# Optimization experiments

Hardware: AMD Instinct MI355X
Metric: run time of the kernel (lower is better)

## Reference

```python
import jax, jax.numpy as jnp
import numpy as np

N = 4096        # num nodes
D_IN = 256      # input_dim
E_DIM = 512     # quantum_dim
H = 8           # num_heads
HD = E_DIM // H # head_dim
N_EDGES = 131072
N_CELL_TYPES = 50


def setup_inputs() -> dict:
    key = jax.random.key(0)
    ks = jax.random.split(key, 12)
    s_in = 1.0 / np.sqrt(D_IN)
    s_e = 1.0 / np.sqrt(E_DIM)
    f32 = jnp.float32
    return {
        "node_features": jax.random.normal(ks[0], (N, D_IN), f32),
        "edge_index": jax.random.randint(ks[1], (2, N_EDGES), 0, N),
        "cell_types": jax.random.randint(ks[2], (N,), 0, N_CELL_TYPES),
        "Wq": (jax.random.normal(ks[3], (E_DIM, D_IN), f32) * s_in),
        "bq": jnp.zeros((E_DIM,), f32),
        "Wk": (jax.random.normal(ks[4], (E_DIM, D_IN), f32) * s_in),
        "bk": jnp.zeros((E_DIM,), f32),
        "Wv": (jax.random.normal(ks[5], (E_DIM, D_IN), f32) * s_in),
        "bv": jnp.zeros((E_DIM,), f32),
        "bio": (jax.random.normal(ks[6], (E_DIM, E_DIM), f32) * s_e),
        "cell_emb": jax.random.normal(ks[7], (N_CELL_TYPES, E_DIM), f32),
        "in_proj_w": (jax.random.normal(ks[8], (3 * E_DIM, E_DIM), f32) * s_e),
        "in_proj_b": jnp.zeros((3 * E_DIM,), f32),
        "out_w": (jax.random.normal(ks[9], (E_DIM, E_DIM), f32) * s_e),
        "out_b": jnp.zeros((E_DIM,), f32),
    }


def reference(node_features, edge_index, cell_types, Wq, bq, Wk, bk, Wv, bv,
              bio, cell_emb, in_proj_w, in_proj_b, out_w, out_b):
    # projections [N, E_DIM]
    Q = node_features @ Wq.T + bq
    K = node_features @ Wk.T + bk
    V = node_features @ Wv.T + bv
    # biological constraint mixing
    Q = Q @ bio
    K = K @ bio.T
    # cell-type embedding offsets
    ce = cell_emb[cell_types]  # [N, E_DIM]
    Q = Q + 0.1 * ce
    K = K + 0.1 * ce
    # graph edge-masked attention scores [N, N]
    scores = (Q @ K.T) / np.float32(np.sqrt(E_DIM))
    mask = jnp.zeros((N, N), jnp.bool_).at[edge_index[0], edge_index[1]].set(True)
    scores = jnp.where(mask, scores, jnp.float32(-1e9))
    attn = jax.nn.softmax(scores, axis=-1)
    # standard MHA (entanglement_layer) in eval mode (no dropout)
    wq_i, wk_i, wv_i = jnp.split(in_proj_w, 3, axis=0)
    bq_i, bk_i, bv_i = jnp.split(in_proj_b, 3)
    q = (Q @ wq_i.T + bq_i).reshape(N, H, HD).transpose(1, 0, 2)  # [H,N,HD]
    k = (K @ wk_i.T + bk_i).reshape(N, H, HD).transpose(1, 0, 2)
    v = (V @ wv_i.T + bv_i).reshape(N, H, HD).transpose(1, 0, 2)
    a2 = jax.nn.softmax(jnp.einsum('hnd,hmd->hnm', q, k) / np.float32(np.sqrt(HD)), axis=-1)
    o = jnp.einsum('hnm,hmd->hnd', a2, v).transpose(1, 0, 2).reshape(N, E_DIM)
    attended = o @ out_w.T + out_b
    # quantum stats
    phase = jnp.arctan2(K, Q)  # angle of complex(Q, K)
    entropy = -jnp.sum(attn * jnp.log(attn + 1e-10))
    coherence = 1.0 - entropy / np.float32(np.log(N))
    return attended, attn, phase, coherence
```

## Files before the change

### kernel.cpp

```cpp
#include <hip/hip_runtime.h>
#include <hip/hip_bf16.h>
#include <math.h>

#define N_NODES 4096
#define DIN     256
#define E       512
#define NH      8
#define HD      64
#define NEDGE   131072
#define MAXE    1024

typedef short bf16x8 __attribute__((ext_vector_type(8)));
typedef float f32x4  __attribute__((ext_vector_type(4)));

__device__ inline short f2bf(float f) {
    __hip_bfloat16 h = __float2bfloat16(f);
    return __builtin_bit_cast(short, h);
}
__device__ inline float bfbits2f(short s) {
    return __bfloat162float(__builtin_bit_cast(__hip_bfloat16, s));
}
__device__ inline void dec2(float f, short& h, short& l) {
    h = f2bf(f);
    l = f2bf(f - bfbits2f(h));
}

__global__ __launch_bounds__(256)
void tr512_k(const float* __restrict__ in, float* __restrict__ out)
{
    __shared__ float Ts[64][65];
    const int x0 = blockIdx.x * 64, y0 = blockIdx.y * 64;
    const int c = threadIdx.x & 63, r0 = threadIdx.x >> 6;
    #pragma unroll
    for (int i = 0; i < 16; ++i) {
        const int r = i * 4 + r0;
        Ts[r][c] = in[(size_t)(y0 + r) * E + x0 + c];
    }
    __syncthreads();
    #pragma unroll
    for (int i = 0; i < 16; ++i) {
        const int r = i * 4 + r0;
        out[(size_t)(x0 + r) * E + y0 + c] = Ts[c][r];
    }
}

__global__ __launch_bounds__(256)
void prep_gemm_k(const float* __restrict__ bio, const float* __restrict__ bioT,
                 const float* __restrict__ ipw,
                 const float* __restrict__ Wq, const float* __restrict__ Wk,
                 const float* __restrict__ Wv,
                 short* __restrict__ Whi, short* __restrict__ Wlo)
{
    const int z = blockIdx.z;
    const float* A = (z == 0) ? bioT : (z == 1) ? bio : (ipw + (size_t)2 * E * E);
    const float* B = (z == 0) ? Wq : (z == 1) ? Wk : Wv;

    __shared__ float As[16][68];
    __shared__ float Bs[16][68];

    const int t  = threadIdx.x;
    const int m0 = blockIdx.y * 64;
    const int n0 = blockIdx.x * 64;
    const int ty = t >> 4, tx = t & 15;

    float acc[4][4] = {{0.f}};

    for (int kt = 0; kt < E; kt += 16) {
        {
            const int row = t >> 2, kq = (t & 3) << 2;
            const float4 va = *(const float4*)(A + (size_t)(m0 + row) * E + kt + kq);
            As[kq + 0][row] = va.x; As[kq + 1][row] = va.y;
            As[kq + 2][row] = va.z; As[kq + 3][row] = va.w;
        }
        {
            const int kk = t >> 4, nq = (t & 15) << 2;
            *(float4*)&Bs[kk][nq] = *(const float4*)(B + (size_t)(kt + kk) * DIN + n0 + nq);
        }
        __syncthreads();
        #pragma unroll
        for (int k = 0; k < 16; ++k) {
            const float4 av = *(const float4*)&As[k][ty << 2];
            const float4 bv = *(const float4*)&Bs[k][tx << 2];
            const float a[4] = {av.x, av.y, av.z, av.w};
            const float b[4] = {bv.x, bv.y, bv.z, bv.w};
            #pragma unroll
            for (int i = 0; i < 4; ++i)
                #pragma unroll
                for (int j = 0; j < 4; ++j)
                    acc[i][j] = fmaf(a[i], b[j], acc[i][j]);
        }
        __syncthreads();
    }

    #pragma unroll
    for (int i = 0; i < 4; ++i) {
        const int row = z * E + m0 + (ty << 2) + i;
        const int col = n0 + (tx << 2);
        #pragma unroll
        for (int j = 0; j < 4; ++j) {
            short h, l;
            dec2(acc[i][j], h, l);
            Whi[(size_t)row * DIN + col + j] = h;
            Wlo[(size_t)row * DIN + col + j] = l;
        }
    }
}

__global__ __launch_bounds__(256)
void bias_prep_k(const float* __restrict__ bq, const float* __restrict__ bk,
                 const float* __restrict__ bv, const float* __restrict__ bio,
                 const float* __restrict__ ipw, const float* __restrict__ ipb,
                 float* __restrict__ beff)
{
    const int n = blockIdx.x * 256 + threadIdx.x;
    float s = 0.f;
    if (n < 512) {
        for (int e = 0; e < E; ++e) s += bq[e] * bio[(size_t)e * E + n];
    } else if (n < 1024) {
        const int nn = n - 512;
        for (int e = 0; e < E; ++e) s += bk[e] * bio[(size_t)nn * E + e];
    } else {
        const int nn = n - 1024;
        const float* wvi = ipw + (size_t)2 * E * E + (size_t)nn * E;
        for (int e = 0; e < E; ++e) s += bv[e] * wvi[e];
        s += ipb[1024 + nn];
    }
    beff[n] = s;
}

__global__ __launch_bounds__(256)
void conv_b16_k(const float* __restrict__ src, short* __restrict__ dst)
{
    const size_t i = ((size_t)blockIdx.x * 256 + threadIdx.x) * 4;
    const float4 v = *(const float4*)(src + i);
    short4 o; o.x = f2bf(v.x); o.y = f2bf(v.y); o.z = f2bf(v.z); o.w = f2bf(v.w);
    *(short4*)(dst + i) = o;
}

__global__ __launch_bounds__(256)
void dec_split_k(const float* __restrict__ src, short* __restrict__ hi,
                 short* __restrict__ lo)
{
    const size_t i = ((size_t)blockIdx.x * 256 + threadIdx.x) * 4;
    const float4 v = *(const float4*)(src + i);
    short4 h, l;
    dec2(v.x, h.x, l.x); dec2(v.y, h.y, l.y);
    dec2(v.z, h.z, l.z); dec2(v.w, h.w, l.w);
    *(short4*)(hi + i) = h;
    *(short4*)(lo + i) = l;
}

template<bool SPLIT, int EPI>
__global__ __launch_bounds__(256)
void mf_gemm_k(const short* __restrict__ Ah, const short* __restrict__ Al,
               const short* __restrict__ Bh, const short* __restrict__ Bl,
               int K,
               const float* __restrict__ beff, const float* __restrict__ cemb,
               const int* __restrict__ ctype,
               float* __restrict__ f32a, float* __restrict__ f32b,
               float* __restrict__ f32c,
               short* __restrict__ b16a, short* __restrict__ b16b)
{
    constexpr int NSL = SPLIT ? 2 : 1;
    __shared__ __align__(16) short As[NSL][128 * 64];
    __shared__ __align__(16) short Bs[NSL][128 * 64];

    const int t = threadIdx.x;
    const int w = t >> 6, lane = t & 63;
    const int quad = lane >> 4, l16 = lane & 15;
    const int m0 = blockIdx.y * 128, n0 = blockIdx.x * 128;
    const int mw = (w >> 1) * 64, nw = (w & 1) * 64;

    const short* Ause = Ah;
    const short* Buse = Bh;
    const float* biasu = beff;
    short* dstu = b16a;
    if (EPI == 1 && blockIdx.z == 1) {
        Ause = Al; Buse = Bh + (size_t)E * E; biasu = beff + E; dstu = b16b;
    }

    f32x4 acc[4][4];
    #pragma unroll
    for (int i = 0; i < 4; ++i)
        #pragma unroll
        for (int j = 0; j < 4; ++j) acc[i][j] = (f32x4){0.f, 0.f, 0.f, 0.f};

    for (int kt = 0; kt < K; kt += 64) {
        __syncthreads();
        #pragma unroll
        for (int it = 0; it < 4; ++it) {
            const int idx = it * 256 + t;
            const int row = idx >> 3, ch = idx & 7;
            const int lo = row * 64 + ((ch ^ (row & 7)) << 3);
            *(bf16x8*)&As[0][lo] = *(const bf16x8*)(Ause + (size_t)(m0 + row) * K + kt + ch * 8);
            *(bf16x8*)&Bs[0][lo] = *(const bf16x8*)(Buse + (size_t)(n0 + row) * K + kt + ch * 8);
            if (SPLIT) {
                *(bf16x8*)&As[1][lo] = *(const bf16x8*)(Al + (size_t)(m0 + row) * K + kt + ch * 8);
                *(bf16x8*)&Bs[1][lo] = *(const bf16x8*)(Bl + (size_t)(n0 + row) * K + kt + ch * 8);
            }
        }
        __syncthreads();

        #pragma unroll
        for (int kk = 0; kk < 2; ++kk) {
            bf16x8 af[4], bf_[4], afl[4], bfl[4];
            #pragma unroll
            for (int i = 0; i < 4; ++i) {
                const int lo = (mw + 16 * i + l16) * 64 + (((kk * 4 + quad) ^ (l16 & 7)) << 3);
                af[i] = *(const bf16x8*)&As[0][lo];
                if (SPLIT) afl[i] = *(const bf16x8*)&As[1][lo];
            }
            #pragma unroll
            for (int j = 0; j < 4; ++j) {
                const int lo = (nw + 16 * j + l16) * 64 + (((kk * 4 + quad) ^ (l16 & 7)) << 3);
                bf_[j] = *(const bf16x8*)&Bs[0][lo];
                if (SPLIT) bfl[j] = *(const bf16x8*)&Bs[1][lo];
            }
            #pragma unroll
            for (int i = 0; i < 4; ++i)
                #pragma unroll
                for (int j = 0; j < 4; ++j) {
                    acc[i][j] = __builtin_amdgcn_mfma_f32_16x16x32_bf16(af[i], bf_[j], acc[i][j], 0, 0, 0);
                    if (SPLIT) {
                        acc[i][j] = __builtin_amdgcn_mfma_f32_16x16x32_bf16(af[i], bfl[j], acc[i][j], 0, 0, 0);
                        acc[i][j] = __builtin_amdgcn_mfma_f32_16x16x32_bf16(afl[i], bf_[j], acc[i][j], 0, 0, 0);
                    }
                }
        }
    }

    #pragma unroll
    for (int i = 0; i < 4; ++i)
        #pragma unroll
        for (int r = 0; r < 4; ++r) {
            const int row = m0 + mw + 16 * i + quad * 4 + r;
            #pragma unroll
            for (int j = 0; j < 4; ++j) {
                const int col = n0 + nw + 16 * j + l16;
                float v = acc[i][j][r];
                if (EPI == 0) {
                    v += beff[col];
                    if (col < 1024) {
                        const int cc = col & 511;
                        v += 0.1f * cemb[(size_t)ctype[row] * E + cc];
                        if (col < 512) {
                            f32a[(size_t)row * E + cc] = v;
                            b16a[(size_t)row * E + cc] = f2bf(v);
                        } else {
                            f32b[(size_t)row * E + cc] = v;
                            b16b[(size_t)row * E + cc] = f2bf(v);
                        }
                    } else {
                        f32c[(size_t)row * E + (col - 1024)] = v;
                    }
                } else if (EPI == 1) {
                    v += biasu[col];
                    dstu[((size_t)(col >> 6) * N_NODES + row) * HD + (col & 63)] = f2bf(v);
                } else {
                    v += biasu[col];
                    f32a[(size_t)row * E + col] = v;
                }
            }
        }
}

__global__ __launch_bounds__(256)
void conv_vt_k(const float* __restrict__ src, short* __restrict__ dst)
{
    __shared__ short Ts[64][72];
    const int h  = blockIdx.x & 7;
    const int n0 = (blockIdx.x >> 3) * 64;
    const int t  = threadIdx.x;
    {
        const int r = t >> 2, s0 = (t & 3) * 16;
        #pragma unroll
        for (int i = 0; i < 4; ++i) {
            const float4 v = *(const float4*)(src + (size_t)(n0 + r) * E + h * HD + s0 + i * 4);
            Ts[r][s0 + i*4 + 0] = f2bf(v.x); Ts[r][s0 + i*4 + 1] = f2bf(v.y);
            Ts[r][s0 + i*4 + 2] = f2bf(v.z); Ts[r][s0 + i*4 + 3] = f2bf(v.w);
        }
    }
    __syncthreads();
    {
        const int d = t >> 2, ns = (t & 3) * 16;
        bf16x8 a, b;
        #pragma unroll
        for (int j = 0; j < 8; ++j) { a[j] = Ts[ns + j][d]; b[j] = Ts[ns + 8 + j][d]; }
        short* o = dst + (size_t)h * HD * N_NODES + (size_t)d * N_NODES + n0 + ns;
        *(bf16x8*)o = a;
        *(bf16x8*)(o + 8) = b;
    }
}

__global__ __launch_bounds__(256)
void flash_mha_k(const short* __restrict__ qh, const short* __restrict__ kh,
                 const short* __restrict__ vt, float* __restrict__ Opart,
                 float* __restrict__ Mpart, float* __restrict__ Lpart)
{
    const int h = blockIdx.y, z = blockIdx.z;
    const int q0 = blockIdx.x * 64;
    const int t = threadIdx.x, wave = t >> 6, lane = t & 63;
    const int quad = lane >> 4, l16 = lane & 15;
    const int sw = l16 & 7;

    __shared__ __align__(16) short Kt[64 * 64];
    __shared__ __align__(16) short Vs[64 * 64];
    __shared__ __align__(16) short Pt[4][16 * 64];

    const short* qb = qh + ((size_t)h * N_NODES + q0 + wave * 16 + l16) * HD;
    const bf16x8 aq0 = *(const bf16x8*)(qb + quad * 8);
    const bf16x8 aq1 = *(const bf16x8*)(qb + 32 + quad * 8);

    f32x4 O[4];
    #pragma unroll
    for (int c = 0; c < 4; ++c) O[c] = (f32x4){0.f, 0.f, 0.f, 0.f};
    float mr = -INFINITY, lr = 0.f;

    const short* kb = kh + (size_t)h * N_NODES * HD;
    const short* vb = vt + (size_t)h * HD * N_NODES;
    const int c0 = (quad ^ sw) << 3;
    const int c1 = c0 ^ 32;

    const int kbeg = z * (N_NODES / 2);
    for (int k0 = kbeg; k0 < kbeg + N_NODES / 2; k0 += 64) {
        __syncthreads();
        #pragma unroll
        for (int it = 0; it < 2; ++it) {
            const int idx = it * 256 + t;
            const int row = idx >> 3, ch = idx & 7;
            const int lo = row * 64 + ((ch ^ (row & 7)) << 3);
            *(bf16x8*)&Kt[lo] = *(const bf16x8*)(kb + (size_t)(k0 + row) * HD + ch * 8);
            *(bf16x8*)&Vs[lo] = *(const bf16x8*)(vb + (size_t)row * N_NODES + k0 + ch * 8);
        }
        __syncthreads();

        f32x4 S[4];
        #pragma unroll
        for (int c = 0; c < 4; ++c) {
            const int rb = (16 * c + l16) * 64;
            const bf16x8 kf0 = *(const bf16x8*)&Kt[rb + c0];
            const bf16x8 kf1 = *(const bf16x8*)&Kt[rb + c1];
            f32x4 a = {0.f, 0.f, 0.f, 0.f};
            a = __builtin_amdgcn_mfma_f32_16x16x32_bf16(kf0, aq0, a, 0, 0, 0);
            a = __builtin_amdgcn_mfma_f32_16x16x32_bf16(kf1, aq1, a, 0, 0, 0);
            S[c] = a * 0.125f;
        }

        float tmax = S[0][0];
        #pragma unroll
        for (int c = 0; c < 4; ++c)
            #pragma unroll
            for (int r = 0; r < 4; ++r) tmax = fmaxf(tmax, S[c][r]);
        tmax = fmaxf(tmax, __shfl_xor(tmax, 16));
        tmax = fmaxf(tmax, __shfl_xor(tmax, 32));

        const float mn = fmaxf(mr, tmax);
        const float alpha = __expf(mr - mn);
        mr = mn;
        float ps = 0.f;
        #pragma unroll
        for (int c = 0; c < 4; ++c)
            #pragma unroll
            for (int r = 0; r < 4; ++r) {
                const float p = __expf(S[c][r] - mn);
                S[c][r] = p;
                ps += p;
            }
        ps += __shfl_xor(ps, 16);
        ps += __shfl_xor(ps, 32);
        lr = lr * alpha + ps;

        float arow[4];
        #pragma unroll
        for (int r = 0; r < 4; ++r)
            arow[r] = __shfl(alpha, (lane & 48) | (((lane >> 2) & 12) + r));
        #pragma unroll
        for (int c = 0; c < 4; ++c)
            #pragma unroll
            for (int r = 0; r < 4; ++r) O[c][r] *= arow[r];

        #pragma unroll
        for (int c = 0; c < 4; ++c)
            #pragma unroll
            for (int r = 0; r < 4; ++r) {
                const int col = 16 * c + quad * 4 + r;
                Pt[wave][l16 * 64 + (((col >> 3) ^ sw) << 3) + (col & 7)] = f2bf(S[c][r]);
            }
        const bf16x8 pf0 = *(const bf16x8*)&Pt[wave][l16 * 64 + c0];
        const bf16x8 pf1 = *(const bf16x8*)&Pt[wave][l16 * 64 + c1];
        #pragma unroll
        for (int c = 0; c < 4; ++c) {
            const int rb = (16 * c + l16) * 64;
            const bf16x8 vf0 = *(const bf16x8*)&Vs[rb + c0];
            const bf16x8 vf1 = *(const bf16x8*)&Vs[rb + c1];
            O[c] = __builtin_amdgcn_mfma_f32_16x16x32_bf16(pf0, vf0, O[c], 0, 0, 0);
            O[c] = __builtin_amdgcn_mfma_f32_16x16x32_bf16(pf1, vf1, O[c], 0, 0, 0);
        }
    }

    const size_t zb = ((size_t)z * NH + h) * N_NODES;
    #pragma unroll
    for (int c = 0; c < 4; ++c)
        #pragma unroll
        for (int r = 0; r < 4; ++r)
            Opart[(zb + q0 + wave * 16 + quad * 4 + r) * HD + 16 * c + l16] = O[c][r];
    if (quad == 0) {
        Mpart[zb + q0 + wave * 16 + l16] = mr;
        Lpart[zb + q0 + wave * 16 + l16] = lr;
    }
}

__global__ __launch_bounds__(256)
void combine_k(const float* __restrict__ Opart, const float* __restrict__ Mp,
               const float* __restrict__ Lp, short* __restrict__ obf)
{
    const int idx = blockIdx.x * 256 + threadIdx.x;
    const int e4 = idx * 4;
    const int q = e4 >> 9;
    const int col = e4 & 511;
    const int h = col >> 6, d = col & 63;
    const size_t b0 = (size_t)h * N_NODES + q;
    const size_t b1 = (size_t)NH * N_NODES + b0;
    const float m0 = Mp[b0], m1 = Mp[b1];
    const float l0 = Lp[b0], l1 = Lp[b1];
    const float M = fmaxf(m0, m1);
    const float w0 = __expf(m0 - M), w1 = __expf(m1 - M);
    const float inv = 1.0f / (w0 * l0 + w1 * l1);
    const float4 o0 = *(const float4*)&Opart[b0 * HD + d];
    const float4 o1 = *(const float4*)&Opart[b1 * HD + d];
    short4 o;
    o.x = f2bf((w0 * o0.x + w1 * o1.x) * inv);
    o.y = f2bf((w0 * o0.y + w1 * o1.y) * inv);
    o.z = f2bf((w0 * o0.z + w1 * o1.z) * inv);
    o.w = f2bf((w0 * o0.w + w1 * o1.w) * inv);
    *(short4*)&obf[(size_t)q * E + col] = o;
}

__global__ __launch_bounds__(256)
void mask_build_k(const int* __restrict__ ei, unsigned* __restrict__ mask)
{
    const int i = blockIdx.x * 256 + threadIdx.x;
    const int r = ei[i];
    const int c = ei[NEDGE + i];
    atomicOr(&mask[(size_t)r * (N_NODES / 32) + (c >> 5)], 1u << (c & 31));
}

__device__ inline float waveMax(float v) {
    #pragma unroll
    for (int o = 32; o; o >>= 1) v = fmaxf(v, __shfl_xor(v, o));
    return v;
}
__device__ inline float waveSum(float v) {
    #pragma unroll
    for (int o = 32; o; o >>= 1) v += __shfl_xor(v, o);
    return v;
}

__global__ __launch_bounds__(256)
void edge_attn_k(const float* __restrict__ Q, const float* __restrict__ Km,
                 const unsigned* __restrict__ mask, float* __restrict__ attn,
                 float* __restrict__ entAcc)
{
    const int row = blockIdx.x;
    const int t = threadIdx.x;
    const int wave = t >> 6, lane = t & 63;
    const size_t rowbase = (size_t)row * N_NODES;

    __shared__ float qrow[E];
    __shared__ int cols[MAXE];
    __shared__ float sc[MAXE];
    __shared__ int cnt;
    __shared__ float red[4];

    {
        const float4 zv = {0.f, 0.f, 0.f, 0.f};
        #pragma unroll
        for (int j = 0; j < 4; ++j)
            *(float4*)&attn[rowbase + j * 1024 + t * 4] = zv;
    }
    qrow[t] = Q[(size_t)row * E + t];
    qrow[256 + t] = Q[(size_t)row * E + 256 + t];
    if (t == 0) cnt = 0;
    __syncthreads();

    if (t < 128) {
        unsigned wm = mask[(size_t)row * (N_NODES / 32) + t];
        while (wm) {
            const int b = __ffs(wm) - 1;
            wm &= wm - 1;
            const int idx = atomicAdd(&cnt, 1);
            cols[idx] = t * 32 + b;
        }
    }
    __syncthreads();
    const int nE = cnt;

    if (nE == 0) {
        const float p = 1.0f / 4096.0f;
        for (int j = t; j < N_NODES; j += 256) attn[rowbase + j] = p;
        if (t == 0) atomicAdd(entAcc, -4096.f * p * logf(p + 1e-10f));
        return;
    }

    const float scale = 0.044194173824159216f;
    for (int e = wave; e < nE; e += 4) {
        const float* kr = Km + (size_t)cols[e] * E;
        float acc = 0.f;
        #pragma unroll
        for (int i = 0; i < 2; ++i) {
            const float4 kv = *(const float4*)(kr + i * 256 + lane * 4);
            const float4 qv = *(const float4*)(&qrow[i * 256 + lane * 4]);
            acc += kv.x * qv.x + kv.y * qv.y + kv.z * qv.z + kv.w * qv.w;
        }
        acc = waveSum(acc);
        if (lane == 0) sc[e] = acc * scale;
    }
    __syncthreads();

    float lm = -3.4e38f;
    for (int e = t; e < nE; e += 256) lm = fmaxf(lm, sc[e]);
    lm = waveMax(lm);
    if (lane == 0) red[wave] = lm;
    __syncthreads();
    const float m = fmaxf(fmaxf(red[0], red[1]), fmaxf(red[2], red[3]));
    __syncthreads();

    float ls = 0.f;
    for (int e = t; e < nE; e += 256) ls += expf(sc[e] - m);
    ls = waveSum(ls);
    if (lane == 0) red[wave] = ls;
    __syncthreads();
    const float inv = 1.0f / (red[0] + red[1] + red[2] + red[3]);
    __syncthreads();

    float ent = 0.f;
    for (int e = t; e < nE; e += 256) {
        const float p = expf(sc[e] - m) * inv;
        attn[rowbase + cols[e]] = p;
        ent -= p * logf(p + 1e-10f);
    }
    ent = waveSum(ent);
    if (lane == 0) red[wave] = ent;
    __syncthreads();
    if (t == 0) atomicAdd(entAcc, red[0] + red[1] + red[2] + red[3]);
}

__global__ __launch_bounds__(256)
void phase_k(const float* __restrict__ Q, const float* __restrict__ K,
             float* __restrict__ out)
{
    const size_t i = (size_t)blockIdx.x * 256 + threadIdx.x;
    out[i] = atan2f(K[i], Q[i]);
}

__global__ void coh_k(const float* __restrict__ ent, float* __restrict__ out)
{
    out[0] = 1.0f - ent[0] / logf(4096.0f);
}

extern "C" void kernel_launch(void* const* d_in, const int* in_sizes, int n_in,
                              void* d_out, int out_size, void* d_ws, size_t ws_size,
                              hipStream_t stream)
{
    const float* x    = (const float*)d_in[0];
    const int*   ei   = (const int*)  d_in[1];
    const int*   ct   = (const int*)  d_in[2];
    const float* Wq   = (const float*)d_in[3];
    const float* bq   = (const float*)d_in[4];
    const float* Wk   = (const float*)d_in[5];
    const float* bk   = (const float*)d_in[6];
    const float* Wv   = (const float*)d_in[7];
    const float* bv   = (const float*)d_in[8];
    const float* bio  = (const float*)d_in[9];
    const float* cemb = (const float*)d_in[10];
    const float* ipw  = (const float*)d_in[11];
    const float* ipb  = (const float*)d_in[12];
    const float* ow   = (const float*)d_in[13];
    const float* ob   = (const float*)d_in[14];

    const size_t NE = (size_t)N_NODES * E;

    float* Qf = (float*)d_ws;
    float* Kf = Qf + NE;
    unsigned* mask = (unsigned*)(Kf + NE);
    float* entAcc = (float*)(mask + (size_t)N_NODES * (N_NODES / 32));

    float* outAttended = (float*)d_out;
    float* outAttn  = outAttended + NE;
    float* outPhase = outAttn + (size_t)N_NODES * N_NODES;
    float* outCoh   = outPhase + NE;

    float* Opart = outAttn;
    float* Mpart = outAttn + 4194304;
    float* Lpart = outAttn + 4259840;
    short* obf   = (short*)(outAttn + 4325376);
    short* vt    = (short*)(outAttn + 5373952);
    short* qh    = (short*)(outAttn + 6422528);
    short* kh    = (short*)(outAttn + 7471104);
    short* Qbf   = (short*)(outAttn + 8519680);
    short* Kbf   = (short*)(outAttn + 9568256);
    short* xhi   = (short*)(outAttn + 10616832);
    short* xlo   = (short*)(outAttn + 11141120);
    short* Wthi  = (short*)(outAttn + 11665408);
    short* Wtlo  = (short*)(outAttn + 11862016);
    short* ipwbf = (short*)(outAttn + 12058624);
    short* owbf  = (short*)(outAttn + 12320768);
    float* bioT  = outAttn + 12451840;
    float* beff  = outAttn + 12713984;
    float* vbuf  = outPhase;

    const dim3 blk(256);

    hipMemsetAsync(mask, 0, (size_t)N_NODES * (N_NODES / 32) * sizeof(unsigned), stream);
    hipMemsetAsync(entAcc, 0, sizeof(float), stream);
    mask_build_k<<<dim3(NEDGE / 256), blk, 0, stream>>>(ei, mask);

    tr512_k<<<dim3(8, 8), blk, 0, stream>>>(bio, bioT);
    prep_gemm_k<<<dim3(4, 8, 3), blk, 0, stream>>>(bio, bioT, ipw, Wq, Wk, Wv, Wthi, Wtlo);
    bias_prep_k<<<dim3(6), blk, 0, stream>>>(bq, bk, bv, bio, ipw, ipb, beff);

    dec_split_k<<<dim3(1024), blk, 0, stream>>>(x, xhi, xlo);
    conv_b16_k<<<dim3(512), blk, 0, stream>>>(ipw, ipwbf);
    conv_b16_k<<<dim3(256), blk, 0, stream>>>(ow, owbf);

    mf_gemm_k<true, 0><<<dim3(12, 32, 1), blk, 0, stream>>>(
        xhi, xlo, Wthi, Wtlo, DIN, beff, cemb, ct,
        Qf, Kf, vbuf, Qbf, Kbf);

    conv_vt_k<<<dim3(512), blk, 0, stream>>>(vbuf, vt);

    mf_gemm_k<false, 1><<<dim3(4, 32, 2), blk, 0, stream>>>(
        Qbf, Kbf, ipwbf, nullptr, E, ipb, nullptr, nullptr,
        nullptr, nullptr, nullptr, qh, kh);

    flash_mha_k<<<dim3(N_NODES / 64, NH, 2), blk, 0, stream>>>(qh, kh, vt, Opart, Mpart, Lpart);
    combine_k<<<dim3((unsigned)(NE / 4 / 256)), blk, 0, stream>>>(Opart, Mpart, Lpart, obf);

    mf_gemm_k<false, 2><<<dim3(4, 32, 1), blk, 0, stream>>>(
        obf, nullptr, owbf, nullptr, E, ob, nullptr, nullptr,
        outAttended, nullptr, nullptr, nullptr, nullptr);

    phase_k<<<dim3((unsigned)(NE / 256)), blk, 0, stream>>>(Qf, Kf, outPhase);

    edge_attn_k<<<dim3(N_NODES), blk, 0, stream>>>(Qf, Kf, mask, outAttn, entAcc);

    coh_k<<<1, 1, 0, stream>>>(entAcc, outCoh);
}
```

Measured before the change: 398.5 us.

## Fuse prep kernels, write V transposed in GEMM epilogue, double-buffer flash attention

Measured after the change: 394.6 us. About the same (-1.0%).

```diff
diff --git a/kernel.cpp b/kernel.cpp
--- a/kernel.cpp
+++ b/kernel.cpp
@@ -9,6 +9,7 @@
 #define HD      64
 #define NEDGE   131072
 #define MAXE    1024
+#define LSC     0.180336880111120f
 
 typedef short bf16x8 __attribute__((ext_vector_type(8)));
 typedef float f32x4  __attribute__((ext_vector_type(4)));
@@ -24,35 +25,19 @@
     h = f2bf(f);
     l = f2bf(f - bfbits2f(h));
 }
-
-__global__ __launch_bounds__(256)
-void tr512_k(const float* __restrict__ in, float* __restrict__ out)
-{
-    __shared__ float Ts[64][65];
-    const int x0 = blockIdx.x * 64, y0 = blockIdx.y * 64;
-    const int c = threadIdx.x & 63, r0 = threadIdx.x >> 6;
-    #pragma unroll
-    for (int i = 0; i < 16; ++i) {
-        const int r = i * 4 + r0;
-        Ts[r][c] = in[(size_t)(y0 + r) * E + x0 + c];
-    }
-    __syncthreads();
-    #pragma unroll
-    for (int i = 0; i < 16; ++i) {
-        const int r = i * 4 + r0;
-        out[(size_t)(x0 + r) * E + y0 + c] = Ts[c][r];
-    }
-}
-
-__global__ __launch_bounds__(256)
-void prep_gemm_k(const float* __restrict__ bio, const float* __restrict__ bioT,
-                 const float* __restrict__ ipw,
+__device__ inline unsigned packbf2(float a, float b) {
+    return (unsigned)(unsigned short)f2bf(a) |
+           ((unsigned)(unsigned short)f2bf(b) << 16);
+}
+
+__global__ __launch_bounds__(256)
+void prep_gemm_k(const float* __restrict__ bio, const float* __restrict__ ipw,
                  const float* __restrict__ Wq, const float* __restrict__ Wk,
                  const float* __restrict__ Wv,
                  short* __restrict__ Whi, short* __restrict__ Wlo)
 {
     const int z = blockIdx.z;
-    const float* A = (z == 0) ? bioT : (z == 1) ? bio : (ipw + (size_t)2 * E * E);
+    const float* A = (z == 2) ? (ipw + (size_t)2 * E * E) : bio;
     const float* B = (z == 0) ? Wq : (z == 1) ? Wk : Wv;
 
     __shared__ float As[16][68];
@@ -66,7 +51,10 @@
     float acc[4][4] = {{0.f}};
 
     for (int kt = 0; kt < E; kt += 16) {
-        {
+        if (z == 0) {
+            const int kk = t >> 4, nq = (t & 15) << 2;
+            *(float4*)&As[kk][nq] = *(const float4*)(A + (size_t)(kt + kk) * E + m0 + nq);
+        } else {
             const int row = t >> 2, kq = (t & 3) << 2;
             const float4 va = *(const float4*)(A + (size_t)(m0 + row) * E + kt + kq);
             As[kq + 0][row] = va.x; As[kq + 1][row] = va.y;
@@ -107,47 +95,50 @@
 }
 
 __global__ __launch_bounds__(256)
-void bias_prep_k(const float* __restrict__ bq, const float* __restrict__ bk,
-                 const float* __restrict__ bv, const float* __restrict__ bio,
-                 const float* __restrict__ ipw, const float* __restrict__ ipb,
-                 float* __restrict__ beff)
-{
-    const int n = blockIdx.x * 256 + threadIdx.x;
-    float s = 0.f;
-    if (n < 512) {
-        for (int e = 0; e < E; ++e) s += bq[e] * bio[(size_t)e * E + n];
-    } else if (n < 1024) {
-        const int nn = n - 512;
-        for (int e = 0; e < E; ++e) s += bk[e] * bio[(size_t)nn * E + e];
+void conv_all_k(const float* __restrict__ x, const float* __restrict__ ipw,
+                const float* __restrict__ ow,
+                const float* __restrict__ bq, const float* __restrict__ bk,
+                const float* __restrict__ bv, const float* __restrict__ bio,
+                const float* __restrict__ ipb,
+                short* __restrict__ xhi, short* __restrict__ xlo,
+                short* __restrict__ ipwbf, short* __restrict__ owbf,
+                float* __restrict__ beff)
+{
+    const int b = blockIdx.x, t = threadIdx.x;
+    if (b < 1024) {
+        const size_t i = ((size_t)b * 256 + t) * 4;
+        const float4 v = *(const float4*)(x + i);
+        short4 h, l;
+        dec2(v.x, h.x, l.x); dec2(v.y, h.y, l.y);
+        dec2(v.z, h.z, l.z); dec2(v.w, h.w, l.w);
+        *(short4*)(xhi + i) = h;
+        *(short4*)(xlo + i) = l;
+    } else if (b < 1536) {
+        const size_t i = ((size_t)(b - 1024) * 256 + t) * 4;
+        const float4 v = *(const float4*)(ipw + i);
+        short4 o; o.x = f2bf(v.x); o.y = f2bf(v.y); o.z = f2bf(v.z); o.w = f2bf(v.w);
+        *(short4*)(ipwbf + i) = o;
+    } else if (b < 1792) {
+        const size_t i = ((size_t)(b - 1536) * 256 + t) * 4;
+        const float4 v = *(const float4*)(ow + i);
+        short4 o; o.x = f2bf(v.x); o.y = f2bf(v.y); o.z = f2bf(v.z); o.w = f2bf(v.w);
+        *(short4*)(owbf + i) = o;
     } else {
-        const int nn = n - 1024;
-        const float* wvi = ipw + (size_t)2 * E * E + (size_t)nn * E;
-        for (int e = 0; e < E; ++e) s += bv[e] * wvi[e];
-        s += ipb[1024 + nn];
-    }
-    beff[n] = s;
-}
-
-__global__ __launch_bounds__(256)
-void conv_b16_k(const float* __restrict__ src, short* __restrict__ dst)
-{
-    const size_t i = ((size_t)blockIdx.x * 256 + threadIdx.x) * 4;
-    const float4 v = *(const float4*)(src + i);
-    short4 o; o.x = f2bf(v.x); o.y = f2bf(v.y); o.z = f2bf(v.z); o.w = f2bf(v.w);
-    *(short4*)(dst + i) = o;
-}
-
-__global__ __launch_bounds__(256)
-void dec_split_k(const float* __restrict__ src, short* __restrict__ hi,
-                 short* __restrict__ lo)
-{
-    const size_t i = ((size_t)blockIdx.x * 256 + threadIdx.x) * 4;
-    const float4 v = *(const float4*)(src + i);
-    short4 h, l;
-    dec2(v.x, h.x, l.x); dec2(v.y, h.y, l.y);
-    dec2(v.z, h.z, l.z); dec2(v.w, h.w, l.w);
-    *(short4*)(hi + i) = h;
-    *(short4*)(lo + i) = l;
+        const int n = (b - 1792) * 256 + t;
+        float s = 0.f;
+        if (n < 512) {
+            for (int e = 0; e < E; ++e) s += bq[e] * bio[(size_t)e * E + n];
+        } else if (n < 1024) {
+            const int nn = n - 512;
+            for (int e = 0; e < E; ++e) s += bk[e] * bio[(size_t)nn * E + e];
+        } else {
+            const int nn = n - 1024;
+            const float* wvi = ipw + (size_t)2 * E * E + (size_t)nn * E;
+            for (int e = 0; e < E; ++e) s += bv[e] * wvi[e];
+            s += ipb[1024 + nn];
+        }
+        beff[n] = s;
+    }
 }
 
 template<bool SPLIT, int EPI>
@@ -158,8 +149,8 @@
                const float* __restrict__ beff, const float* __restrict__ cemb,
                const int* __restrict__ ctype,
                float* __restrict__ f32a, float* __restrict__ f32b,
-               float* __restrict__ f32c,
-               short* __restrict__ b16a, short* __restrict__ b16b)
+               short* __restrict__ b16a, short* __restrict__ b16b,
+               short* __restrict__ b16c)
 {
     constexpr int NSL = SPLIT ? 2 : 1;
     __shared__ __align__(16) short As[NSL][128 * 64];
@@ -230,28 +221,35 @@
     }
 
     #pragma unroll
-    for (int i = 0; i < 4; ++i)
-        #pragma unroll
-        for (int r = 0; r < 4; ++r) {
-            const int row = m0 + mw + 16 * i + quad * 4 + r;
-            #pragma unroll
-            for (int j = 0; j < 4; ++j) {
-                const int col = n0 + nw + 16 * j + l16;
+    for (int i = 0; i < 4; ++i) {
+        const int row0 = m0 + mw + 16 * i + quad * 4;
+        #pragma unroll
+        for (int j = 0; j < 4; ++j) {
+            const int col = n0 + nw + 16 * j + l16;
+            if (EPI == 0 && col >= 1024) {
+                const int hh = (col - 1024) >> 6, d = (col - 1024) & 63;
+                short4 o;
+                o.x = f2bf(acc[i][j][0] + beff[col]);
+                o.y = f2bf(acc[i][j][1] + beff[col]);
+                o.z = f2bf(acc[i][j][2] + beff[col]);
+                o.w = f2bf(acc[i][j][3] + beff[col]);
+                *(short4*)(b16c + ((size_t)hh * HD + d) * N_NODES + row0) = o;
+                continue;
+            }
+            #pragma unroll
+            for (int r = 0; r < 4; ++r) {
+                const int row = row0 + r;
                 float v = acc[i][j][r];
                 if (EPI == 0) {
                     v += beff[col];
-                    if (col < 1024) {
-                        const int cc = col & 511;
-                        v += 0.1f * cemb[(size_t)ctype[row] * E + cc];
-                        if (col < 512) {
-                            f32a[(size_t)row * E + cc] = v;
-                            b16a[(size_t)row * E + cc] = f2bf(v);
-                        } else {
-                            f32b[(size_t)row * E + cc] = v;
-                            b16b[(size_t)row * E + cc] = f2bf(v);
-                        }
+                    const int cc = col & 511;
+                    v += 0.1f * cemb[(size_t)ctype[row] * E + cc];
+                    if (col < 512) {
+                        f32a[(size_t)row * E + cc] = v;
+                        b16a[(size_t)row * E + cc] = f2bf(v);
                     } else {
-                        f32c[(size_t)row * E + (col - 1024)] = v;
+                        f32b[(size_t)row * E + cc] = v;
+                        b16b[(size_t)row * E + cc] = f2bf(v);
                     }
                 } else if (EPI == 1) {
                     v += biasu[col];
@@ -262,33 +260,6 @@
                 }
             }
         }
-}
-
-__global__ __launch_bounds__(256)
-void conv_vt_k(const float* __restrict__ src, short* __restrict__ dst)
-{
-    __shared__ short Ts[64][72];
-    const int h  = blockIdx.x & 7;
-    const int n0 = (blockIdx.x >> 3) * 64;
-    const int t  = threadIdx.x;
-    {
-        const int r = t >> 2, s0 = (t & 3) * 16;
-        #pragma unroll
-        for (int i = 0; i < 4; ++i) {
-            const float4 v = *(const float4*)(src + (size_t)(n0 + r) * E + h * HD + s0 + i * 4);
-            Ts[r][s0 + i*4 + 0] = f2bf(v.x); Ts[r][s0 + i*4 + 1] = f2bf(v.y);
-            Ts[r][s0 + i*4 + 2] = f2bf(v.z); Ts[r][s0 + i*4 + 3] = f2bf(v.w);
-        }
-    }
-    __syncthreads();
-    {
-        const int d = t >> 2, ns = (t & 3) * 16;
-        bf16x8 a, b;
-        #pragma unroll
-        for (int j = 0; j < 8; ++j) { a[j] = Ts[ns + j][d]; b[j] = Ts[ns + 8 + j][d]; }
-        short* o = dst + (size_t)h * HD * N_NODES + (size_t)d * N_NODES + n0 + ns;
-        *(bf16x8*)o = a;
-        *(bf16x8*)(o + 8) = b;
     }
 }
 
@@ -303,8 +274,8 @@
     const int quad = lane >> 4, l16 = lane & 15;
     const int sw = l16 & 7;
 
-    __shared__ __align__(16) short Kt[64 * 64];
-    __shared__ __align__(16) short Vs[64 * 64];
+    __shared__ __align__(16) short Kt[2][64 * 64];
+    __shared__ __align__(16) short Vs[2][64 * 64];
     __shared__ __align__(16) short Pt[4][16 * 64];
 
     const short* qb = qh + ((size_t)h * N_NODES + q0 + wave * 16 + l16) * HD;
@@ -321,29 +292,50 @@
     const int c0 = (quad ^ sw) << 3;
     const int c1 = c0 ^ 32;
 
+    int rows[2], chs[2], los[2];
+    #pragma unroll
+    for (int it = 0; it < 2; ++it) {
+        const int idx = it * 256 + t;
+        rows[it] = idx >> 3; chs[it] = idx & 7;
+        los[it] = rows[it] * 64 + ((chs[it] ^ (rows[it] & 7)) << 3);
+    }
+
     const int kbeg = z * (N_NODES / 2);
-    for (int k0 = kbeg; k0 < kbeg + N_NODES / 2; k0 += 64) {
-        __syncthreads();
-        #pragma unroll
-        for (int it = 0; it < 2; ++it) {
-            const int idx = it * 256 + t;
-            const int row = idx >> 3, ch = idx & 7;
-            const int lo = row * 64 + ((ch ^ (row & 7)) << 3);
-            *(bf16x8*)&Kt[lo] = *(const bf16x8*)(kb + (size_t)(k0 + row) * HD + ch * 8);
-            *(bf16x8*)&Vs[lo] = *(const bf16x8*)(vb + (size_t)row * N_NODES + k0 + ch * 8);
-        }
-        __syncthreads();
+    bf16x8 pk[2], pv[2];
+    #pragma unroll
+    for (int it = 0; it < 2; ++it) {
+        pk[it] = *(const bf16x8*)(kb + (size_t)(kbeg + rows[it]) * HD + chs[it] * 8);
+        pv[it] = *(const bf16x8*)(vb + (size_t)rows[it] * N_NODES + kbeg + chs[it] * 8);
+    }
+    #pragma unroll
+    for (int it = 0; it < 2; ++it) {
+        *(bf16x8*)&Kt[0][los[it]] = pk[it];
+        *(bf16x8*)&Vs[0][los[it]] = pv[it];
+    }
+    __syncthreads();
+
+    const int NT = (N_NODES / 2) / 64;
+    for (int i = 0; i < NT; ++i) {
+        const int cur = i & 1;
+        if (i + 1 < NT) {
+            const int nxt = kbeg + (i + 1) * 64;
+            #pragma unroll
+            for (int it = 0; it < 2; ++it) {
+                pk[it] = *(const bf16x8*)(kb + (size_t)(nxt + rows[it]) * HD + chs[it] * 8);
+                pv[it] = *(const bf16x8*)(vb + (size_t)rows[it] * N_NODES + nxt + chs[it] * 8);
+            }
+        }
 
         f32x4 S[4];
         #pragma unroll
         for (int c = 0; c < 4; ++c) {
             const int rb = (16 * c + l16) * 64;
-            const bf16x8 kf0 = *(const bf16x8*)&Kt[rb + c0];
-            const bf16x8 kf1 = *(const bf16x8*)&Kt[rb + c1];
+            const bf16x8 kf0 = *(const bf16x8*)&Kt[cur][rb + c0];
+            const bf16x8 kf1 = *(const bf16x8*)&Kt[cur][rb + c1];
             f32x4 a = {0.f, 0.f, 0.f, 0.f};
             a = __builtin_amdgcn_mfma_f32_16x16x32_bf16(kf0, aq0, a, 0, 0, 0);
             a = __builtin_amdgcn_mfma_f32_16x16x32_bf16(kf1, aq1, a, 0, 0, 0);
-            S[c] = a * 0.125f;
+            S[c] = a;
         }
 
         float tmax = S[0][0];
@@ -355,14 +347,15 @@
         tmax = fmaxf(tmax, __shfl_xor(tmax, 32));
 
         const float mn = fmaxf(mr, tmax);
-        const float alpha = __expf(mr - mn);
+        const float alpha = exp2f((mr - mn) * LSC);
         mr = mn;
+        const float cc = -mn * LSC;
         float ps = 0.f;
         #pragma unroll
         for (int c = 0; c < 4; ++c)
             #pragma unroll
             for (int r = 0; r < 4; ++r) {
-                const float p = __expf(S[c][r] - mn);
+                const float p = exp2f(fmaf(S[c][r], LSC, cc));
                 S[c][r] = p;
                 ps += p;
             }
@@ -380,22 +373,31 @@
             for (int r = 0; r < 4; ++r) O[c][r] *= arow[r];
 
         #pragma unroll
-        for (int c = 0; c < 4; ++c)
-            #pragma unroll
-            for (int r = 0; r < 4; ++r) {
-                const int col = 16 * c + quad * 4 + r;
-                Pt[wave][l16 * 64 + (((col >> 3) ^ sw) << 3) + (col & 7)] = f2bf(S[c][r]);
-            }
+        for (int c = 0; c < 4; ++c) {
+            const int chunk = 2 * c + (quad >> 1);
+            const int off = l16 * 64 + ((chunk ^ sw) << 3) + (quad & 1) * 4;
+            *(unsigned*)&Pt[wave][off]     = packbf2(S[c][0], S[c][1]);
+            *(unsigned*)&Pt[wave][off + 2] = packbf2(S[c][2], S[c][3]);
+        }
         const bf16x8 pf0 = *(const bf16x8*)&Pt[wave][l16 * 64 + c0];
         const bf16x8 pf1 = *(const bf16x8*)&Pt[wave][l16 * 64 + c1];
         #pragma unroll
         for (int c = 0; c < 4; ++c) {
             const int rb = (16 * c + l16) * 64;
-            const bf16x8 vf0 = *(const bf16x8*)&Vs[rb + c0];
-            const bf16x8 vf1 = *(const bf16x8*)&Vs[rb + c1];
+            const bf16x8 vf0 = *(const bf16x8*)&Vs[cur][rb + c0];
+            const bf16x8 vf1 = *(const bf16x8*)&Vs[cur][rb + c1];
             O[c] = __builtin_amdgcn_mfma_f32_16x16x32_bf16(pf0, vf0, O[c], 0, 0, 0);
             O[c] = __builtin_amdgcn_mfma_f32_16x16x32_bf16(pf1, vf1, O[c], 0, 0, 0);
         }
+
+        if (i + 1 < NT) {
+            #pragma unroll
+            for (int it = 0; it < 2; ++it) {
+                *(bf16x8*)&Kt[cur ^ 1][los[it]] = pk[it];
+                *(bf16x8*)&Vs[cur ^ 1][los[it]] = pv[it];
+            }
+        }
+        __syncthreads();
     }
 
     const size_t zb = ((size_t)z * NH + h) * N_NODES;
@@ -405,7 +407,7 @@
         for (int r = 0; r < 4; ++r)
             Opart[(zb + q0 + wave * 16 + quad * 4 + r) * HD + 16 * c + l16] = O[c][r];
     if (quad == 0) {
-        Mpart[zb + q0 + wave * 16 + l16] = mr;
+        Mpart[zb + q0 + wave * 16 + l16] = mr * LSC;
         Lpart[zb + q0 + wave * 16 + l16] = lr;
     }
 }
@@ -424,7 +426,7 @@
     const float m0 = Mp[b0], m1 = Mp[b1];
     const float l0 = Lp[b0], l1 = Lp[b1];
     const float M = fmaxf(m0, m1);
-    const float w0 = __expf(m0 - M), w1 = __expf(m1 - M);
+    const float w0 = exp2f(m0 - M), w1 = exp2f(m1 - M);
     const float inv = 1.0f / (w0 * l0 + w1 * l1);
     const float4 o0 = *(const float4*)&Opart[b0 * HD + d];
     const float4 o1 = *(const float4*)&Opart[b1 * HD + d];
@@ -605,33 +607,24 @@
     short* Wtlo  = (short*)(outAttn + 11862016);
     short* ipwbf = (short*)(outAttn + 12058624);
     short* owbf  = (short*)(outAttn + 12320768);
-    float* bioT  = outAttn + 12451840;
     float* beff  = outAttn + 12713984;
-    float* vbuf  = outPhase;
 
     const dim3 blk(256);
 
-    hipMemsetAsync(mask, 0, (size_t)N_NODES * (N_NODES / 32) * sizeof(unsigned), stream);
-    hipMemsetAsync(entAcc, 0, sizeof(float), stream);
+    (void)hipMemsetAsync(mask, 0, (size_t)N_NODES * (N_NODES / 32) * sizeof(unsigned) + 4, stream);
     mask_build_k<<<dim3(NEDGE / 256), blk, 0, stream>>>(ei, mask);
 
-    tr512_k<<<dim3(8, 8), blk, 0, stream>>>(bio, bioT);
-    prep_gemm_k<<<dim3(4, 8, 3), blk, 0, stream>>>(bio, bioT, ipw, Wq, Wk, Wv, Wthi, Wtlo);
-    bias_prep_k<<<dim3(6), blk, 0, stream>>>(bq, bk, bv, bio, ipw, ipb, beff);
-
-    dec_split_k<<<dim3(1024), blk, 0, stream>>>(x, xhi, xlo);
-    conv_b16_k<<<dim3(512), blk, 0, stream>>>(ipw, ipwbf);
-    conv_b16_k<<<dim3(256), blk, 0, stream>>>(ow, owbf);
+    prep_gemm_k<<<dim3(4, 8, 3), blk, 0, stream>>>(bio, ipw, Wq, Wk, Wv, Wthi, Wtlo);
+    conv_all_k<<<dim3(1798), blk, 0, stream>>>(x, ipw, ow, bq, bk, bv, bio, ipb,
+                                               xhi, xlo, ipwbf, owbf, beff);
 
     mf_gemm_k<true, 0><<<dim3(12, 32, 1), blk, 0, stream>>>(
         xhi, xlo, Wthi, Wtlo, DIN, beff, cemb, ct,
-        Qf, Kf, vbuf, Qbf, Kbf);
-
-    conv_vt_k<<<dim3(512), blk, 0, stream>>>(vbuf, vt);
+        Qf, Kf, Qbf, Kbf, vt);
 
     mf_gemm_k<false, 1><<<dim3(4, 32, 2), blk, 0, stream>>>(
         Qbf, Kbf, ipwbf, nullptr, E, ipb, nullptr, nullptr,
-        nullptr, nullptr, nullptr, qh, kh);
+        nullptr, nullptr, qh, kh, nullptr);
 
     flash_mha_k<<<dim3(N_NODES / 64, NH, 2), blk, 0, stream>>>(qh, kh, vt, Opart, Mpart, Lpart);
     combine_k<<<dim3((unsigned)(NE / 4 / 256)), blk, 0, stream>>>(Opart, Mpart, Lpart, obf);
```
